# Optimization experiments

Hardware: AMD Instinct MI355X
Metric: run time of the kernel (lower is better)

Reference implementation:

```python
import jax, jax.numpy as jnp
import numpy as np

N_NODES = 50000
N_EDGES = 800000
FEA_DIM = 128
N_LAYER = 3
ACTOR_H = 512
N_GRAPHS = 64


def gcn_conv(x, src, dst, W, b, n_nodes):
    """PyG GCNConv: add self-loops, symmetric deg normalization, linear, scatter-add.
    out[i] = sum_{j->i} d_j^{-1/2} d_i^{-1/2} (x_j W) + d_i^{-1} (x_i W) + b
    where d_i = in_degree(i) + 1 (self-loop included)."""
    h = x @ W  # [N, F]
    deg = jax.ops.segment_sum(jnp.ones(src.shape[0], x.dtype), dst, num_segments=n_nodes) + 1.0
    dinv = jax.lax.rsqrt(deg)  # [N]
    coef = (dinv[src] * dinv[dst])[:, None]  # [E, 1]
    agg = jax.ops.segment_sum(h[src] * coef, dst, num_segments=n_nodes)  # gather-scale-scatter
    agg = agg + h * (dinv * dinv)[:, None]  # self-loop term
    return agg + b


def setup_inputs() -> dict:
    key = jax.random.key(0)
    ks = jax.random.split(key, 12)
    x = jax.random.normal(ks[0], (N_NODES, FEA_DIM), dtype=jnp.float32)
    edge_index = jax.random.randint(ks[1], (2, N_EDGES), 0, N_NODES, dtype=jnp.int32)
    batch = jnp.sort(jax.random.randint(ks[2], (N_NODES,), 0, N_GRAPHS, dtype=jnp.int32))
    s = 1.0 / np.sqrt(FEA_DIM)
    conv_W = jax.random.normal(ks[3], (N_LAYER, FEA_DIM, FEA_DIM), dtype=jnp.float32) * s
    conv_b = jnp.zeros((N_LAYER, FEA_DIM), dtype=jnp.float32)
    fea_w1 = jax.random.normal(ks[4], (FEA_DIM, ACTOR_H), dtype=jnp.float32) * s
    fea_b1 = jnp.zeros((ACTOR_H,), dtype=jnp.float32)
    fea_w2 = jax.random.normal(ks[5], (ACTOR_H, FEA_DIM), dtype=jnp.float32) * (1.0 / np.sqrt(ACTOR_H))
    fea_b2 = jnp.zeros((FEA_DIM,), dtype=jnp.float32)
    node_w = jax.random.normal(ks[6], (FEA_DIM, 1), dtype=jnp.float32) * s
    node_b = jnp.zeros((1,), dtype=jnp.float32)
    return {"x": x, "edge_index": edge_index, "batch": batch,
            "conv_W": conv_W, "conv_b": conv_b,
            "fea_w1": fea_w1, "fea_b1": fea_b1,
            "fea_w2": fea_w2, "fea_b2": fea_b2,
            "node_w": node_w, "node_b": node_b}


def reference(x, edge_index, batch, conv_W, conv_b, fea_w1, fea_b1, fea_w2, fea_b2, node_w, node_b):
    src, dst = edge_index[0], edge_index[1]
    n_nodes = x.shape[0]
    for l in range(N_LAYER):  # fixed small layer loop
        x = jax.nn.relu(gcn_conv(x, src, dst, conv_W[l], conv_b[l], n_nodes))
    node_prob = jnp.squeeze(x @ node_w + node_b, axis=-1)  # [N]
    # global mean pool over graphs
    sums = jax.ops.segment_sum(x, batch, num_segments=N_GRAPHS)  # [G, F]
    cnts = jax.ops.segment_sum(jnp.ones(n_nodes, x.dtype), batch, num_segments=N_GRAPHS)
    fea = sums / jnp.maximum(cnts, 1.0)[:, None]
    fea = jax.nn.relu(fea @ fea_w1 + fea_b1)
    fea_prob = fea @ fea_w2 + fea_b2  # [G, F]
    return (node_prob, fea_prob)
```

## Files before the change

kernel.cpp:

```cpp
#include <hip/hip_runtime.h>

#define N_NODES 50000
#define N_EDGES 800000
#define FEA 128
#define NL 3
#define AH 512
#define NG 64
#define NBLK 196

typedef short bf16x8 __attribute__((ext_vector_type(8)));
typedef float f32x4 __attribute__((ext_vector_type(4)));
typedef uint  u32x4 __attribute__((ext_vector_type(4)));

__device__ __forceinline__ ushort f2bf(float f) {
    uint u = __float_as_uint(f);
    uint r = u + 0x7FFFu + ((u >> 16) & 1u);
    return (ushort)(r >> 16);
}
__device__ __forceinline__ float bf2f(ushort u) {
    return __uint_as_float((uint)u << 16);
}

__global__ void k_deg(const int* __restrict__ dst, int* __restrict__ deg,
                      ushort* __restrict__ rank) {
    int i = blockIdx.x * blockDim.x + threadIdx.x;
    if (i < N_EDGES) rank[i] = (ushort)atomicAdd(&deg[dst[i]], 1);
}

__device__ __forceinline__ int block_scan_incl(int v, int* wsum) {
    int lane = threadIdx.x & 63, w = threadIdx.x >> 6;
    int s = v;
#pragma unroll
    for (int off = 1; off < 64; off <<= 1) {
        int t = __shfl_up(s, off);
        if (lane >= off) s += t;
    }
    if (lane == 63) wsum[w] = s;
    __syncthreads();
    int woff = 0;
    for (int k = 0; k < w; ++k) woff += wsum[k];
    return woff + s;
}

__global__ __launch_bounds__(256) void k_scan1(const int* __restrict__ deg,
                                               int* __restrict__ rowptr,
                                               int* __restrict__ bsum,
                                               float* __restrict__ dinv) {
    __shared__ int wsum[4];
    int i = blockIdx.x * 256 + threadIdx.x;
    int v = (i < N_NODES) ? deg[i] : 0;
    int pv = (v + 7) & ~7;
    int incl = block_scan_incl(pv, wsum);
    if (i < N_NODES) {
        rowptr[i] = incl - pv;
        dinv[i] = rsqrtf((float)v + 1.0f);
    }
    if (threadIdx.x == 255) bsum[blockIdx.x] = incl;
}

__global__ __launch_bounds__(256) void k_scan2(int* __restrict__ bsum,
                                               int* __restrict__ boff,
                                               int* __restrict__ rowptr) {
    __shared__ int wsum[4];
    int v = (threadIdx.x < NBLK) ? bsum[threadIdx.x] : 0;
    int incl = block_scan_incl(v, wsum);
    if (threadIdx.x < NBLK) boff[threadIdx.x] = incl - v;
    if (threadIdx.x == NBLK - 1) rowptr[N_NODES] = incl;
}

__global__ __launch_bounds__(256) void k_scan3(int* __restrict__ rowptr,
                                               const int* __restrict__ boff) {
    int i = blockIdx.x * 256 + threadIdx.x;
    if (i < N_NODES) rowptr[i] += boff[blockIdx.x];
}

__global__ void k_fill(const int* __restrict__ src, const int* __restrict__ dst,
                       const int* __restrict__ rowptr, const ushort* __restrict__ rank,
                       ushort* __restrict__ eidx) {
    int e = blockIdx.x * blockDim.x + threadIdx.x;
    if (e < N_EDGES) eidx[rowptr[dst[e]] + (int)rank[e]] = (ushort)src[e];
}

#define PA 6250
#define PB (PA + NBLK)
#define PC (PB + NBLK)
#define PD (PC + 512)
#define PE (PD + 192)
#define PF (PE + 1)
__global__ __launch_bounds__(256) void k_prep(const float* __restrict__ x,
                                              const int* __restrict__ batch,
                                              const int* __restrict__ deg,
                                              const int* __restrict__ rowptr,
                                              const float* __restrict__ convW,
                                              const float* __restrict__ w1,
                                              const float* __restrict__ w2,
                                              ushort* __restrict__ eidx,
                                              int* __restrict__ gstart,
                                              ushort* __restrict__ Xhi,
                                              ushort* __restrict__ Xlo,
                                              ushort* __restrict__ WhiT,
                                              ushort* __restrict__ WloT,
                                              float* __restrict__ w1T,
                                              float* __restrict__ w2T,
                                              ushort* __restrict__ H) {
    int blk = blockIdx.x;
    if (blk < PA) {
        int i4 = blk * 1024 + threadIdx.x * 4;
        float4 v = *(const float4*)(x + i4);
        ushort h0 = f2bf(v.x), h1 = f2bf(v.y), h2 = f2bf(v.z), h3 = f2bf(v.w);
        uint2 hv, lv;
        hv.x = (uint)h0 | ((uint)h1 << 16);
        hv.y = (uint)h2 | ((uint)h3 << 16);
        lv.x = (uint)f2bf(v.x - bf2f(h0)) | ((uint)f2bf(v.y - bf2f(h1)) << 16);
        lv.y = (uint)f2bf(v.z - bf2f(h2)) | ((uint)f2bf(v.w - bf2f(h3)) << 16);
        *(uint2*)(Xhi + i4) = hv;
        *(uint2*)(Xlo + i4) = lv;
    } else if (blk < PB) {
        int i = (blk - PA) * 256 + threadIdx.x;
        if (i < N_NODES) {
            int d = deg[i], r = rowptr[i];
            int pd = (d + 7) & ~7;
            for (int k = d; k < pd; ++k) eidx[r + k] = (ushort)N_NODES;
        }
    } else if (blk < PC) {
        int i = (blk - PB) * 256 + threadIdx.x;
        if (i < N_NODES) {
            int b = batch[i];
            int bp = (i == 0) ? -1 : batch[i - 1];
            for (int g = bp + 1; g <= b; ++g) gstart[g] = i;
            if (i == N_NODES - 1)
                for (int g = b + 1; g <= NG; ++g) gstart[g] = N_NODES;
        }
    } else if (blk < PD) {
        int idx = (blk - PC) * 256 + threadIdx.x;
        if (idx < FEA * AH) {
            int k = idx >> 9, j = idx & 511;
            w1T[(size_t)j * FEA + k] = w1[idx];
        } else {
            int t = idx - FEA * AH;
            int k = t >> 7, f = t & 127;
            w2T[(size_t)f * AH + k] = w2[t];
        }
    } else if (blk < PE) {
        int t = (blk - PD) * 256 + threadIdx.x;
        int l = t >> 14, r = t & 16383;
        int k = r >> 7, c = r & 127;
        float w = convW[t];
        ushort h = f2bf(w);
        WhiT[(size_t)l * 16384 + c * FEA + k] = h;
        WloT[(size_t)l * 16384 + c * FEA + k] = f2bf(w - bf2f(h));
    } else {
        if (threadIdx.x < 64) ((uint*)(H + (size_t)N_NODES * FEA))[threadIdx.x] = 0;
    }
}

__global__ __launch_bounds__(256) void k_gemm(const ushort* __restrict__ Xhi,
                                              const ushort* __restrict__ Xlo,
                                              const ushort* __restrict__ WhiT,
                                              const ushort* __restrict__ WloT,
                                              const float* __restrict__ dinv,
                                              ushort* __restrict__ H) {
    const int wv = threadIdx.x >> 6;
    const int lane = threadIdx.x & 63;
    const int lr = lane & 15;
    const int lk = lane >> 4;

    bf16x8 bhi[2][4], blo[2][4];
#pragma unroll
    for (int ct = 0; ct < 2; ++ct) {
        int col = wv * 32 + ct * 16 + lr;
#pragma unroll
        for (int kf = 0; kf < 4; ++kf) {
            bhi[ct][kf] = *(const bf16x8*)(WhiT + (size_t)col * FEA + kf * 32 + lk * 8);
            blo[ct][kf] = *(const bf16x8*)(WloT + (size_t)col * FEA + kf * 32 + lk * 8);
        }
    }

    for (int rt = blockIdx.x; rt < N_NODES / 16; rt += gridDim.x) {
        int r0 = rt * 16;
        const ushort* xh = Xhi + (size_t)(r0 + lr) * FEA;
        const ushort* xl = Xlo + (size_t)(r0 + lr) * FEA;
        bf16x8 ahi[4], alo[4];
#pragma unroll
        for (int kf = 0; kf < 4; ++kf) {
            ahi[kf] = *(const bf16x8*)(xh + kf * 32 + lk * 8);
            alo[kf] = *(const bf16x8*)(xl + kf * 32 + lk * 8);
        }
        f32x4 acc0 = {0.f, 0.f, 0.f, 0.f};
        f32x4 acc1 = {0.f, 0.f, 0.f, 0.f};
#pragma unroll
        for (int kf = 0; kf < 4; ++kf) {
            acc0 = __builtin_amdgcn_mfma_f32_16x16x32_bf16(ahi[kf], bhi[0][kf], acc0, 0, 0, 0);
            acc0 = __builtin_amdgcn_mfma_f32_16x16x32_bf16(ahi[kf], blo[0][kf], acc0, 0, 0, 0);
            acc0 = __builtin_amdgcn_mfma_f32_16x16x32_bf16(alo[kf], bhi[0][kf], acc0, 0, 0, 0);
            acc1 = __builtin_amdgcn_mfma_f32_16x16x32_bf16(ahi[kf], bhi[1][kf], acc1, 0, 0, 0);
            acc1 = __builtin_amdgcn_mfma_f32_16x16x32_bf16(ahi[kf], blo[1][kf], acc1, 0, 0, 0);
            acc1 = __builtin_amdgcn_mfma_f32_16x16x32_bf16(alo[kf], bhi[1][kf], acc1, 0, 0, 0);
        }
#pragma unroll
        for (int reg = 0; reg < 4; ++reg) {
            int orow = r0 + lk * 4 + reg;
            float s = dinv[orow];
            H[(size_t)orow * FEA + wv * 32 + lr]      = f2bf(acc0[reg] * s);
            H[(size_t)orow * FEA + wv * 32 + 16 + lr] = f2bf(acc1[reg] * s);
        }
    }
}

__global__ __launch_bounds__(256) void k_gather(const int* __restrict__ rowptr,
                                                const ushort* __restrict__ eidx,
                                                const float* __restrict__ dinv,
                                                const ushort* __restrict__ H,
                                                const float* __restrict__ b,
                                                ushort* __restrict__ Xhi,
                                                ushort* __restrict__ Xlo,
                                                const float* __restrict__ nw,
                                                const float* __restrict__ nbp,
                                                float* __restrict__ out_node,
                                                int last) {
    int t = blockIdx.x * 256 + threadIdx.x;
    int node = t >> 4;
    int c8 = t & 15;
    if (node >= N_NODES) return;
    const uint4* H4 = (const uint4*)H;
    int r0 = rowptr[node], r1 = rowptr[node + 1];

    float a[8] = {0.f, 0.f, 0.f, 0.f, 0.f, 0.f, 0.f, 0.f};
#define ACC8(u)                                                              \
    do {                                                                     \
        a[0] += __uint_as_float((u).x << 16);                                \
        a[1] += __uint_as_float((u).x & 0xffff0000u);                        \
        a[2] += __uint_as_float((u).y << 16);                                \
        a[3] += __uint_as_float((u).y & 0xffff0000u);                        \
        a[4] += __uint_as_float((u).z << 16);                                \
        a[5] += __uint_as_float((u).z & 0xffff0000u);                        \
        a[6] += __uint_as_float((u).w << 16);                                \
        a[7] += __uint_as_float((u).w & 0xffff0000u);                        \
    } while (0)

    uint4 sv = H4[(size_t)node * 16 + c8];
    ACC8(sv);

    for (int j = r0; j < r1; j += 8) {
        int s0 = eidx[j + 0], s1 = eidx[j + 1];
        int s2 = eidx[j + 2], s3 = eidx[j + 3];
        int s4 = eidx[j + 4], s5 = eidx[j + 5];
        int s6 = eidx[j + 6], s7 = eidx[j + 7];
        uint4 h0 = H4[(size_t)s0 * 16 + c8];
        uint4 h1 = H4[(size_t)s1 * 16 + c8];
        uint4 h2 = H4[(size_t)s2 * 16 + c8];
        uint4 h3 = H4[(size_t)s3 * 16 + c8];
        uint4 h4 = H4[(size_t)s4 * 16 + c8];
        uint4 h5 = H4[(size_t)s5 * 16 + c8];
        uint4 h6 = H4[(size_t)s6 * 16 + c8];
        uint4 h7 = H4[(size_t)s7 * 16 + c8];
        ACC8(h0); ACC8(h1); ACC8(h2); ACC8(h3);
        ACC8(h4); ACC8(h5); ACC8(h6); ACC8(h7);
    }
#undef ACC8

    float di = dinv[node];
    const float4* b4 = (const float4*)b;
    float4 bb0 = b4[c8 * 2], bb1 = b4[c8 * 2 + 1];
    float o[8];
    o[0] = fmaxf(a[0] * di + bb0.x, 0.f);
    o[1] = fmaxf(a[1] * di + bb0.y, 0.f);
    o[2] = fmaxf(a[2] * di + bb0.z, 0.f);
    o[3] = fmaxf(a[3] * di + bb0.w, 0.f);
    o[4] = fmaxf(a[4] * di + bb1.x, 0.f);
    o[5] = fmaxf(a[5] * di + bb1.y, 0.f);
    o[6] = fmaxf(a[6] * di + bb1.z, 0.f);
    o[7] = fmaxf(a[7] * di + bb1.w, 0.f);

    if (last) {
        const float4* nw4 = (const float4*)nw;
        float4 n0 = nw4[c8 * 2], n1 = nw4[c8 * 2 + 1];
        float dot = o[0] * n0.x + o[1] * n0.y + o[2] * n0.z + o[3] * n0.w
                  + o[4] * n1.x + o[5] * n1.y + o[6] * n1.z + o[7] * n1.w;
        dot += __shfl_xor(dot, 1);
        dot += __shfl_xor(dot, 2);
        dot += __shfl_xor(dot, 4);
        dot += __shfl_xor(dot, 8);
        if (c8 == 0) out_node[node] = dot + nbp[0];
    }

    ushort hs[8];
    uint ls[8];
#pragma unroll
    for (int i = 0; i < 8; ++i) {
        hs[i] = f2bf(o[i]);
        ls[i] = f2bf(o[i] - bf2f(hs[i]));
    }
    u32x4 hv, lv;
    hv.x = (uint)hs[0] | ((uint)hs[1] << 16);
    hv.y = (uint)hs[2] | ((uint)hs[3] << 16);
    hv.z = (uint)hs[4] | ((uint)hs[5] << 16);
    hv.w = (uint)hs[6] | ((uint)hs[7] << 16);
    lv.x = ls[0] | (ls[1] << 16);
    lv.y = ls[2] | (ls[3] << 16);
    lv.z = ls[4] | (ls[5] << 16);
    lv.w = ls[6] | (ls[7] << 16);
    __builtin_nontemporal_store(hv, (u32x4*)(Xhi + (size_t)node * FEA + c8 * 8));
    __builtin_nontemporal_store(lv, (u32x4*)(Xlo + (size_t)node * FEA + c8 * 8));
}

__global__ __launch_bounds__(256) void k_pool(const ushort* __restrict__ Xhi,
                                              const ushort* __restrict__ Xlo,
                                              const int* __restrict__ gstart,
                                              float* __restrict__ psum_part) {
    int g = blockIdx.x >> 4, p = blockIdx.x & 15;
    int s = gstart[g], e = gstart[g + 1];
    int len = e - s;
    int lp = (len + 15) >> 4;
    int ps = s + p * lp, pe = min(ps + lp, e);
    int q = threadIdx.x >> 6, lane = threadIdx.x & 63;
    float2 acc = {0.f, 0.f};
    for (int node = ps + q; node < pe; node += 4) {
        uint hv = *(const uint*)(Xhi + (size_t)node * FEA + lane * 2);
        uint lv = *(const uint*)(Xlo + (size_t)node * FEA + lane * 2);
        acc.x += bf2f((ushort)hv) + bf2f((ushort)lv);
        acc.y += bf2f((ushort)(hv >> 16)) + bf2f((ushort)(lv >> 16));
    }
    __shared__ float lds[4 * FEA];
    lds[q * FEA + lane * 2 + 0] = acc.x;
    lds[q * FEA + lane * 2 + 1] = acc.y;
    __syncthreads();
    if (threadIdx.x < FEA) {
        psum_part[(size_t)blockIdx.x * FEA + threadIdx.x] =
            lds[threadIdx.x] + lds[FEA + threadIdx.x] +
            lds[2 * FEA + threadIdx.x] + lds[3 * FEA + threadIdx.x];
    }
}

__global__ __launch_bounds__(256) void k_mlp1(const float* __restrict__ psum_part,
                                              const int* __restrict__ gstart,
                                              const float* __restrict__ w1T,
                                              const float* __restrict__ b1,
                                              float* __restrict__ h1ws) {
    __shared__ float feas[NG * 132];
    for (int idx = threadIdx.x; idx < NG * FEA; idx += 256) {
        int g = idx >> 7, f = idx & 127;
        const float* pp = psum_part + (size_t)g * 16 * FEA + f;
        float sum = 0.f;
#pragma unroll
        for (int p = 0; p < 16; ++p) sum += pp[p * FEA];
        float cnt = fmaxf((float)(gstart[g + 1] - gstart[g]), 1.0f);
        feas[g * 132 + f] = sum / cnt;
    }
    __syncthreads();
    int g = threadIdx.x >> 2, jj = threadIdx.x & 3;
    int j = blockIdx.x * 4 + jj;
    const float4* fr = (const float4*)(feas + g * 132);
    const float4* wr = (const float4*)(w1T + (size_t)j * FEA);
    float4 a0 = {0.f, 0.f, 0.f, 0.f}, a1 = {0.f, 0.f, 0.f, 0.f};
#pragma unroll
    for (int i = 0; i < 16; ++i) {
        float4 f0 = fr[2 * i], w0 = wr[2 * i];
        float4 f1 = fr[2 * i + 1], w1v = wr[2 * i + 1];
        a0.x += f0.x * w0.x; a0.y += f0.y * w0.y;
        a0.z += f0.z * w0.z; a0.w += f0.w * w0.w;
        a1.x += f1.x * w1v.x; a1.y += f1.y * w1v.y;
        a1.z += f1.z * w1v.z; a1.w += f1.w * w1v.w;
    }
    float s = (a0.x + a0.y) + (a0.z + a0.w) + (a1.x + a1.y) + (a1.z + a1.w);
    h1ws[(size_t)g * AH + j] = fmaxf(s + b1[j], 0.f);
}

__global__ __launch_bounds__(256) void k_mlp2(const float* __restrict__ h1ws,
                                              const float* __restrict__ w2T,
                                              const float* __restrict__ b2,
                                              float* __restrict__ out_fea) {
    int f = blockIdx.x;
    int g = threadIdx.x >> 2, q = threadIdx.x & 3;
    const float4* hr = (const float4*)(h1ws + (size_t)g * AH + q * 128);
    const float4* wr = (const float4*)(w2T + (size_t)f * AH + q * 128);
    float4 a0 = {0.f, 0.f, 0.f, 0.f}, a1 = {0.f, 0.f, 0.f, 0.f};
#pragma unroll
    for (int i = 0; i < 16; ++i) {
        float4 h0 = hr[2 * i], w0 = wr[2 * i];
        float4 h1 = hr[2 * i + 1], w1v = wr[2 * i + 1];
        a0.x += h0.x * w0.x; a0.y += h0.y * w0.y;
        a0.z += h0.z * w0.z; a0.w += h0.w * w0.w;
        a1.x += h1.x * w1v.x; a1.y += h1.y * w1v.y;
        a1.z += h1.z * w1v.z; a1.w += h1.w * w1v.w;
    }
    float p = (a0.x + a0.y) + (a0.z + a0.w) + (a1.x + a1.y) + (a1.z + a1.w);
    p += __shfl_xor(p, 1);
    p += __shfl_xor(p, 2);
    if (q == 0) out_fea[(size_t)g * FEA + f] = p + b2[f];
}

extern "C" void kernel_launch(void* const* d_in, const int* in_sizes, int n_in,
                              void* d_out, int out_size, void* d_ws, size_t ws_size,
                              hipStream_t stream) {
    const float* x     = (const float*)d_in[0];
    const int*   ei    = (const int*)d_in[1];
    const int*   batch = (const int*)d_in[2];
    const float* convW = (const float*)d_in[3];
    const float* convb = (const float*)d_in[4];
    const float* w1    = (const float*)d_in[5];
    const float* b1    = (const float*)d_in[6];
    const float* w2    = (const float*)d_in[7];
    const float* b2    = (const float*)d_in[8];
    const float* nw    = (const float*)d_in[9];
    const float* nb    = (const float*)d_in[10];
    float* out = (float*)d_out;

    char* wsb = (char*)d_ws;
    int*    deg    = (int*)wsb;
    float*  dinv   = (float*)(wsb + 50048ll * 4);
    int*    rowptr = (int*)(wsb + 100096ll * 4);
    int*    bsum   = (int*)(wsb + 150144ll * 4);
    int*    boff   = (int*)(wsb + 150344ll * 4);
    int*    gstart = (int*)(wsb + 150544ll * 4);
    int*    rankw  = (int*)(wsb + 150656ll * 4);
    ushort* rank   = (ushort*)rankw;
    float*  w1T    = (float*)rankw;
    float*  w2T    = (float*)(rankw + 65536);
    float*  h1ws   = (float*)(rankw + 131072);
    ushort* WhiT   = (ushort*)(rankw + 163840);
    ushort* WloT   = (ushort*)(rankw + 188416);
    ushort* eidx   = (ushort*)(wsb + 950656ll * 4);
    ushort* H      = (ushort*)(wsb + 1600672ll * 4);
    ushort* Xhi    = (ushort*)(wsb + 4800736ll * 4);
    ushort* Xlo    = (ushort*)(wsb + 8000736ll * 4);
    float*  psum_part = (float*)(wsb + 11200736ll * 4);

    const int* srcp = ei;
    const int* dstp = ei + N_EDGES;

    hipMemsetAsync(deg, 0, N_NODES * sizeof(int), stream);
    k_deg<<<(N_EDGES + 255) / 256, 256, 0, stream>>>(dstp, deg, rank);
    k_scan1<<<NBLK, 256, 0, stream>>>(deg, rowptr, bsum, dinv);
    k_scan2<<<1, 256, 0, stream>>>(bsum, boff, rowptr);
    k_scan3<<<NBLK, 256, 0, stream>>>(rowptr, boff);
    k_fill<<<(N_EDGES + 255) / 256, 256, 0, stream>>>(srcp, dstp, rowptr, rank, eidx);
    k_prep<<<PF, 256, 0, stream>>>(x, batch, deg, rowptr, convW, w1, w2,
                                   eidx, gstart, Xhi, Xlo, WhiT, WloT, w1T, w2T, H);

    for (int l = 0; l < NL; ++l) {
        k_gemm<<<1024, 256, 0, stream>>>(Xhi, Xlo, WhiT + (size_t)l * 16384,
                                         WloT + (size_t)l * 16384, dinv, H);
        k_gather<<<(N_NODES * 16 + 255) / 256, 256, 0, stream>>>(
            rowptr, eidx, dinv, H, convb + (size_t)l * FEA, Xhi, Xlo,
            nw, nb, out, l == NL - 1 ? 1 : 0);
    }

    k_pool<<<NG * 16, 256, 0, stream>>>(Xhi, Xlo, gstart, psum_part);
    k_mlp1<<<128, 256, 0, stream>>>(psum_part, gstart, w1T, b1, h1ws);
    k_mlp2<<<128, 256, 0, stream>>>(h1ws, w2T, b2, out + N_NODES);
}
```

Before: 262.4 us.

## Merge preprocessing kernels, drop MLP weight transposes, vectorize neighbor index loads

Folds the x/W bf16 hi-lo split into the degree-counting kernel and merges edge fill with padding and graph-start computation, cutting one launch and letting independent preprocessing overlap with the atomic degree pass. Removes the w1/w2 transpose stage by having the MLP kernels read the original row-major weights with strided access. Loads eight neighbor indices with one 16-byte load in the gather loop. WhiT/WloT now alias the psum_part buffer, which is only written later by the pool kernel, so reuse is safe as long as that ordering holds.

```diff
diff --git a/kernel.cpp b/kernel.cpp
--- a/kernel.cpp
+++ b/kernel.cpp
@@ -21,10 +21,46 @@
     return __uint_as_float((uint)u << 16);
 }
 
-__global__ void k_deg(const int* __restrict__ dst, int* __restrict__ deg,
-                      ushort* __restrict__ rank) {
-    int i = blockIdx.x * blockDim.x + threadIdx.x;
-    if (i < N_EDGES) rank[i] = (ushort)atomicAdd(&deg[dst[i]], 1);
+#define DA 3125
+#define DB (DA + 6250)
+#define DC (DB + 192)
+#define DD (DC + 1)
+__global__ __launch_bounds__(256) void k_deg_prep(const int* __restrict__ dst,
+                                                  int* __restrict__ deg,
+                                                  ushort* __restrict__ rank,
+                                                  const float* __restrict__ x,
+                                                  ushort* __restrict__ Xhi,
+                                                  ushort* __restrict__ Xlo,
+                                                  const float* __restrict__ convW,
+                                                  ushort* __restrict__ WhiT,
+                                                  ushort* __restrict__ WloT,
+                                                  ushort* __restrict__ H) {
+    int blk = blockIdx.x;
+    if (blk < DA) {
+        int i = blk * 256 + threadIdx.x;
+        rank[i] = (ushort)atomicAdd(&deg[dst[i]], 1);
+    } else if (blk < DB) {
+        int i4 = (blk - DA) * 1024 + threadIdx.x * 4;
+        float4 v = *(const float4*)(x + i4);
+        ushort h0 = f2bf(v.x), h1 = f2bf(v.y), h2 = f2bf(v.z), h3 = f2bf(v.w);
+        uint2 hv, lv;
+        hv.x = (uint)h0 | ((uint)h1 << 16);
+        hv.y = (uint)h2 | ((uint)h3 << 16);
+        lv.x = (uint)f2bf(v.x - bf2f(h0)) | ((uint)f2bf(v.y - bf2f(h1)) << 16);
+        lv.y = (uint)f2bf(v.z - bf2f(h2)) | ((uint)f2bf(v.w - bf2f(h3)) << 16);
+        *(uint2*)(Xhi + i4) = hv;
+        *(uint2*)(Xlo + i4) = lv;
+    } else if (blk < DC) {
+        int t = (blk - DB) * 256 + threadIdx.x;
+        int l = t >> 14, r = t & 16383;
+        int k = r >> 7, c = r & 127;
+        float w = convW[t];
+        ushort h = f2bf(w);
+        WhiT[(size_t)l * 16384 + c * FEA + k] = h;
+        WloT[(size_t)l * 16384 + c * FEA + k] = f2bf(w - bf2f(h));
+    } else {
+        if (threadIdx.x < 64) ((uint*)(H + (size_t)N_NODES * FEA))[threadIdx.x] = 0;
+    }
 }
 
 __device__ __forceinline__ int block_scan_incl(int v, int* wsum) {
@@ -74,56 +110,30 @@
     if (i < N_NODES) rowptr[i] += boff[blockIdx.x];
 }
 
-__global__ void k_fill(const int* __restrict__ src, const int* __restrict__ dst,
-                       const int* __restrict__ rowptr, const ushort* __restrict__ rank,
-                       ushort* __restrict__ eidx) {
-    int e = blockIdx.x * blockDim.x + threadIdx.x;
-    if (e < N_EDGES) eidx[rowptr[dst[e]] + (int)rank[e]] = (ushort)src[e];
-}
-
-#define PA 6250
-#define PB (PA + NBLK)
-#define PC (PB + NBLK)
-#define PD (PC + 512)
-#define PE (PD + 192)
-#define PF (PE + 1)
-__global__ __launch_bounds__(256) void k_prep(const float* __restrict__ x,
-                                              const int* __restrict__ batch,
-                                              const int* __restrict__ deg,
-                                              const int* __restrict__ rowptr,
-                                              const float* __restrict__ convW,
-                                              const float* __restrict__ w1,
-                                              const float* __restrict__ w2,
-                                              ushort* __restrict__ eidx,
-                                              int* __restrict__ gstart,
-                                              ushort* __restrict__ Xhi,
-                                              ushort* __restrict__ Xlo,
-                                              ushort* __restrict__ WhiT,
-                                              ushort* __restrict__ WloT,
-                                              float* __restrict__ w1T,
-                                              float* __restrict__ w2T,
-                                              ushort* __restrict__ H) {
+#define FA 3125
+#define FB (FA + NBLK)
+#define FC (FB + NBLK)
+__global__ __launch_bounds__(256) void k_fill2(const int* __restrict__ src,
+                                               const int* __restrict__ dst,
+                                               const int* __restrict__ rowptr,
+                                               const ushort* __restrict__ rank,
+                                               const int* __restrict__ deg,
+                                               const int* __restrict__ batch,
+                                               ushort* __restrict__ eidx,
+                                               int* __restrict__ gstart) {
     int blk = blockIdx.x;
-    if (blk < PA) {
-        int i4 = blk * 1024 + threadIdx.x * 4;
-        float4 v = *(const float4*)(x + i4);
-        ushort h0 = f2bf(v.x), h1 = f2bf(v.y), h2 = f2bf(v.z), h3 = f2bf(v.w);
-        uint2 hv, lv;
-        hv.x = (uint)h0 | ((uint)h1 << 16);
-        hv.y = (uint)h2 | ((uint)h3 << 16);
-        lv.x = (uint)f2bf(v.x - bf2f(h0)) | ((uint)f2bf(v.y - bf2f(h1)) << 16);
-        lv.y = (uint)f2bf(v.z - bf2f(h2)) | ((uint)f2bf(v.w - bf2f(h3)) << 16);
-        *(uint2*)(Xhi + i4) = hv;
-        *(uint2*)(Xlo + i4) = lv;
-    } else if (blk < PB) {
-        int i = (blk - PA) * 256 + threadIdx.x;
+    if (blk < FA) {
+        int e = blk * 256 + threadIdx.x;
+        eidx[rowptr[dst[e]] + (int)rank[e]] = (ushort)src[e];
+    } else if (blk < FB) {
+        int i = (blk - FA) * 256 + threadIdx.x;
         if (i < N_NODES) {
             int d = deg[i], r = rowptr[i];
             int pd = (d + 7) & ~7;
             for (int k = d; k < pd; ++k) eidx[r + k] = (ushort)N_NODES;
         }
-    } else if (blk < PC) {
-        int i = (blk - PB) * 256 + threadIdx.x;
+    } else {
+        int i = (blk - FB) * 256 + threadIdx.x;
         if (i < N_NODES) {
             int b = batch[i];
             int bp = (i == 0) ? -1 : batch[i - 1];
@@ -131,26 +141,6 @@
             if (i == N_NODES - 1)
                 for (int g = b + 1; g <= NG; ++g) gstart[g] = N_NODES;
         }
-    } else if (blk < PD) {
-        int idx = (blk - PC) * 256 + threadIdx.x;
-        if (idx < FEA * AH) {
-            int k = idx >> 9, j = idx & 511;
-            w1T[(size_t)j * FEA + k] = w1[idx];
-        } else {
-            int t = idx - FEA * AH;
-            int k = t >> 7, f = t & 127;
-            w2T[(size_t)f * AH + k] = w2[t];
-        }
-    } else if (blk < PE) {
-        int t = (blk - PD) * 256 + threadIdx.x;
-        int l = t >> 14, r = t & 16383;
-        int k = r >> 7, c = r & 127;
-        float w = convW[t];
-        ushort h = f2bf(w);
-        WhiT[(size_t)l * 16384 + c * FEA + k] = h;
-        WloT[(size_t)l * 16384 + c * FEA + k] = f2bf(w - bf2f(h));
-    } else {
-        if (threadIdx.x < 64) ((uint*)(H + (size_t)N_NODES * FEA))[threadIdx.x] = 0;
     }
 }
 
@@ -242,10 +232,11 @@
     ACC8(sv);
 
     for (int j = r0; j < r1; j += 8) {
-        int s0 = eidx[j + 0], s1 = eidx[j + 1];
-        int s2 = eidx[j + 2], s3 = eidx[j + 3];
-        int s4 = eidx[j + 4], s5 = eidx[j + 5];
-        int s6 = eidx[j + 6], s7 = eidx[j + 7];
+        uint4 ev = *(const uint4*)(eidx + j);
+        int s0 = ev.x & 0xffff, s1 = ev.x >> 16;
+        int s2 = ev.y & 0xffff, s3 = ev.y >> 16;
+        int s4 = ev.z & 0xffff, s5 = ev.z >> 16;
+        int s6 = ev.w & 0xffff, s7 = ev.w >> 16;
         uint4 h0 = H4[(size_t)s0 * 16 + c8];
         uint4 h1 = H4[(size_t)s1 * 16 + c8];
         uint4 h2 = H4[(size_t)s2 * 16 + c8];
@@ -334,7 +325,7 @@
 
 __global__ __launch_bounds__(256) void k_mlp1(const float* __restrict__ psum_part,
                                               const int* __restrict__ gstart,
-                                              const float* __restrict__ w1T,
+                                              const float* __restrict__ w1,
                                               const float* __restrict__ b1,
                                               float* __restrict__ h1ws) {
     __shared__ float feas[NG * 132];
@@ -350,41 +341,35 @@
     __syncthreads();
     int g = threadIdx.x >> 2, jj = threadIdx.x & 3;
     int j = blockIdx.x * 4 + jj;
-    const float4* fr = (const float4*)(feas + g * 132);
-    const float4* wr = (const float4*)(w1T + (size_t)j * FEA);
-    float4 a0 = {0.f, 0.f, 0.f, 0.f}, a1 = {0.f, 0.f, 0.f, 0.f};
-#pragma unroll
-    for (int i = 0; i < 16; ++i) {
-        float4 f0 = fr[2 * i], w0 = wr[2 * i];
-        float4 f1 = fr[2 * i + 1], w1v = wr[2 * i + 1];
-        a0.x += f0.x * w0.x; a0.y += f0.y * w0.y;
-        a0.z += f0.z * w0.z; a0.w += f0.w * w0.w;
-        a1.x += f1.x * w1v.x; a1.y += f1.y * w1v.y;
-        a1.z += f1.z * w1v.z; a1.w += f1.w * w1v.w;
-    }
-    float s = (a0.x + a0.y) + (a0.z + a0.w) + (a1.x + a1.y) + (a1.z + a1.w);
-    h1ws[(size_t)g * AH + j] = fmaxf(s + b1[j], 0.f);
+    const float* fr = feas + g * 132;
+    float a0 = 0.f, a1 = 0.f, a2 = 0.f, a3 = 0.f;
+#pragma unroll 8
+    for (int k = 0; k < FEA; k += 4) {
+        a0 += fr[k + 0] * w1[(k + 0) * AH + j];
+        a1 += fr[k + 1] * w1[(k + 1) * AH + j];
+        a2 += fr[k + 2] * w1[(k + 2) * AH + j];
+        a3 += fr[k + 3] * w1[(k + 3) * AH + j];
+    }
+    h1ws[(size_t)g * AH + j] = fmaxf((a0 + a1) + (a2 + a3) + b1[j], 0.f);
 }
 
 __global__ __launch_bounds__(256) void k_mlp2(const float* __restrict__ h1ws,
-                                              const float* __restrict__ w2T,
+                                              const float* __restrict__ w2,
                                               const float* __restrict__ b2,
                                               float* __restrict__ out_fea) {
     int f = blockIdx.x;
     int g = threadIdx.x >> 2, q = threadIdx.x & 3;
-    const float4* hr = (const float4*)(h1ws + (size_t)g * AH + q * 128);
-    const float4* wr = (const float4*)(w2T + (size_t)f * AH + q * 128);
-    float4 a0 = {0.f, 0.f, 0.f, 0.f}, a1 = {0.f, 0.f, 0.f, 0.f};
-#pragma unroll
-    for (int i = 0; i < 16; ++i) {
-        float4 h0 = hr[2 * i], w0 = wr[2 * i];
-        float4 h1 = hr[2 * i + 1], w1v = wr[2 * i + 1];
-        a0.x += h0.x * w0.x; a0.y += h0.y * w0.y;
-        a0.z += h0.z * w0.z; a0.w += h0.w * w0.w;
-        a1.x += h1.x * w1v.x; a1.y += h1.y * w1v.y;
-        a1.z += h1.z * w1v.z; a1.w += h1.w * w1v.w;
-    }
-    float p = (a0.x + a0.y) + (a0.z + a0.w) + (a1.x + a1.y) + (a1.z + a1.w);
+    const float* hr = h1ws + (size_t)g * AH + q * 128;
+    const float* wr = w2 + (size_t)q * 128 * FEA + f;
+    float a0 = 0.f, a1 = 0.f, a2 = 0.f, a3 = 0.f;
+#pragma unroll 8
+    for (int k = 0; k < 128; k += 4) {
+        a0 += hr[k + 0] * wr[(k + 0) * FEA];
+        a1 += hr[k + 1] * wr[(k + 1) * FEA];
+        a2 += hr[k + 2] * wr[(k + 2) * FEA];
+        a3 += hr[k + 3] * wr[(k + 3) * FEA];
+    }
+    float p = (a0 + a1) + (a2 + a3);
     p += __shfl_xor(p, 1);
     p += __shfl_xor(p, 2);
     if (q == 0) out_fea[(size_t)g * FEA + f] = p + b2[f];
@@ -415,28 +400,24 @@
     int*    gstart = (int*)(wsb + 150544ll * 4);
     int*    rankw  = (int*)(wsb + 150656ll * 4);
     ushort* rank   = (ushort*)rankw;
-    float*  w1T    = (float*)rankw;
-    float*  w2T    = (float*)(rankw + 65536);
-    float*  h1ws   = (float*)(rankw + 131072);
-    ushort* WhiT   = (ushort*)(rankw + 163840);
-    ushort* WloT   = (ushort*)(rankw + 188416);
+    float*  h1ws   = (float*)rankw;
     ushort* eidx   = (ushort*)(wsb + 950656ll * 4);
     ushort* H      = (ushort*)(wsb + 1600672ll * 4);
     ushort* Xhi    = (ushort*)(wsb + 4800736ll * 4);
     ushort* Xlo    = (ushort*)(wsb + 8000736ll * 4);
     float*  psum_part = (float*)(wsb + 11200736ll * 4);
+    ushort* WhiT   = (ushort*)psum_part;
+    ushort* WloT   = WhiT + 49152;
 
     const int* srcp = ei;
     const int* dstp = ei + N_EDGES;
 
     hipMemsetAsync(deg, 0, N_NODES * sizeof(int), stream);
-    k_deg<<<(N_EDGES + 255) / 256, 256, 0, stream>>>(dstp, deg, rank);
+    k_deg_prep<<<DD, 256, 0, stream>>>(dstp, deg, rank, x, Xhi, Xlo, convW, WhiT, WloT, H);
     k_scan1<<<NBLK, 256, 0, stream>>>(deg, rowptr, bsum, dinv);
     k_scan2<<<1, 256, 0, stream>>>(bsum, boff, rowptr);
     k_scan3<<<NBLK, 256, 0, stream>>>(rowptr, boff);
-    k_fill<<<(N_EDGES + 255) / 256, 256, 0, stream>>>(srcp, dstp, rowptr, rank, eidx);
-    k_prep<<<PF, 256, 0, stream>>>(x, batch, deg, rowptr, convW, w1, w2,
-                                   eidx, gstart, Xhi, Xlo, WhiT, WloT, w1T, w2T, H);
+    k_fill2<<<FC, 256, 0, stream>>>(srcp, dstp, rowptr, rank, deg, batch, eidx, gstart);
 
     for (int l = 0; l < NL; ++l) {
         k_gemm<<<1024, 256, 0, stream>>>(Xhi, Xlo, WhiT + (size_t)l * 16384,
@@ -447,6 +428,6 @@
     }
 
     k_pool<<<NG * 16, 256, 0, stream>>>(Xhi, Xlo, gstart, psum_part);
-    k_mlp1<<<128, 256, 0, stream>>>(psum_part, gstart, w1T, b1, h1ws);
-    k_mlp2<<<128, 256, 0, stream>>>(h1ws, w2T, b2, out + N_NODES);
-}
+    k_mlp1<<<128, 256, 0, stream>>>(psum_part, gstart, w1, b1, h1ws);
+    k_mlp2<<<128, 256, 0, stream>>>(h1ws, w2, b2, out + N_NODES);
+}
```

After: 257.0 us. -2.1%, faster.
